# Optimization experiments

Hardware: AMD Instinct MI355X
Metric: run time of the kernel (lower is better)

Reference implementation:

```python
import jax, jax.numpy as jnp
import numpy as np

N_NODES = 100000
N_EDGES = 1600000
D_FEAT = 32


def setup_inputs() -> dict:
    key = jax.random.key(0)
    k1, k2, k3 = jax.random.split(key, 3)
    return {
        "x_real": jax.random.normal(k1, (N_NODES, D_FEAT), dtype=jnp.float32),
        "x_imag": jax.random.normal(k2, (N_NODES, D_FEAT), dtype=jnp.float32),
        "edge_index": jax.random.randint(k3, (2, N_EDGES), 0, N_NODES, dtype=jnp.int64),
        "evolution_time": jnp.asarray(0.5, dtype=jnp.float32),
        "diffusion_strength": jnp.asarray(1.0, dtype=jnp.float32),
    }


def reference(x_real, x_imag, edge_index, evolution_time, diffusion_strength):
    eps = 1e-8
    num_nodes = x_real.shape[0]
    x = x_real + 1j * x_imag  # [N, D] complex64

    # add self loops
    loops = jnp.arange(num_nodes, dtype=edge_index.dtype)
    row = jnp.concatenate([edge_index[0], loops])  # [E+N]
    col = jnp.concatenate([edge_index[1], loops])  # [E+N]

    # symmetric degree normalization: deg computed over col (as in source)
    deg = jnp.zeros((num_nodes,), jnp.float32).at[col].add(1.0)
    deg_inv_sqrt = jnp.where(deg > 0, deg ** -0.5, 0.0)
    norm = (deg_inv_sqrt[row] * deg_inv_sqrt[col])[:, None]  # [E+N, 1]

    def propagate(h):
        # gather by col, scale, scatter-add by row
        msgs = h[col] * norm.astype(h.dtype)
        return jnp.zeros_like(h).at[row].add(msgs)

    first_order = propagate(x)
    coeff1 = 1j * (evolution_time * diffusion_strength)
    evolved = x + coeff1 * first_order

    # evolution_order >= 2 (second-order Taylor term)
    second_order = propagate(first_order)
    evolved = evolved + (coeff1 * coeff1) * 0.5 * second_order

    # per-node |psi|^2 weights, normalized to sum to num_nodes
    w = (evolved * jnp.conj(evolved)).real.sum(axis=-1, keepdims=True)  # [N,1]
    s = w.sum()
    w = jnp.where(s > eps, w / s * num_nodes, jnp.ones_like(w))
    return w, evolved
```

## Files before the change

kernel.cpp:

```cpp
#include <hip/hip_runtime.h>
#include <cstdint>
#include <cstddef>


#define TPB 256
#define BSL 64
#define CRANGE 16384
#define SRANGE 8192

typedef _Float16 h2 __attribute__((ext_vector_type(2)));

#if defined(__has_builtin)
#if __has_builtin(__builtin_amdgcn_fdot2)
#define HAS_FDOT2 1
#endif
#endif

__device__ __forceinline__ h2 u2h(uint32_t u) {
    union { uint32_t u; h2 h; } x; x.u = u; return x.h;
}
__device__ __forceinline__ uint32_t h2u(h2 h) {
    union { uint32_t u; h2 h; } x; x.h = h; return x.u;
}
__device__ __forceinline__ uint32_t packh(float re, float im) {
    h2 h; h.x = (_Float16)re; h.y = (_Float16)im; return h2u(h);
}
__device__ __forceinline__ void acc2(uint32_t p, float& aR, float& aI) {
#ifdef HAS_FDOT2
    h2 v = u2h(p);
    h2 LO; LO.x = (_Float16)1.0f; LO.y = (_Float16)0.0f;
    h2 HI; HI.x = (_Float16)0.0f; HI.y = (_Float16)1.0f;
    aR = __builtin_amdgcn_fdot2(v, LO, aR, false);
    aI = __builtin_amdgcn_fdot2(v, HI, aI, false);
#else
    h2 v = u2h(p);
    aR += (float)v.x;
    aI += (float)v.y;
#endif
}

__device__ __forceinline__ int slice_len(int E) {
    return (((E + BSL - 1) / BSL) + 3) & ~3;
}

__global__ void k_cnt2(const int* __restrict__ col, const int* __restrict__ row,
                       int E, int Nw, uint32_t* __restrict__ parts_col,
                       uint32_t* __restrict__ parts_row) {
    __shared__ uint32_t sh[CRANGE / 2];
    int which = blockIdx.x & 1;
    int rb = blockIdx.x >> 1;
    int r = rb / BSL, b = rb % BSL;
    const int* keys = which ? row : col;
    uint32_t*  parts = which ? parts_row : parts_col;
    int rbase = r * CRANGE;
    for (int i = threadIdx.x; i < CRANGE / 2; i += TPB) sh[i] = 0;
    __syncthreads();
    int SL = slice_len(E);
    int s0 = b * SL, s1 = min(E, s0 + SL);
    int n = s1 - s0;
    if (n > 0) {
        const int4* k4 = (const int4*)(keys + s0);
        int n4 = n >> 2;
        for (int j = threadIdx.x; j < n4; j += TPB) {
            int4 v = k4[j];
            int k;
            k = v.x - rbase; if ((unsigned)k < CRANGE) atomicAdd(&sh[k >> 1], 1u << ((k & 1) * 16));
            k = v.y - rbase; if ((unsigned)k < CRANGE) atomicAdd(&sh[k >> 1], 1u << ((k & 1) * 16));
            k = v.z - rbase; if ((unsigned)k < CRANGE) atomicAdd(&sh[k >> 1], 1u << ((k & 1) * 16));
            k = v.w - rbase; if ((unsigned)k < CRANGE) atomicAdd(&sh[k >> 1], 1u << ((k & 1) * 16));
        }
        for (int e = s0 + (n4 << 2) + threadIdx.x; e < s1; e += TPB) {
            int k = keys[e] - rbase;
            if ((unsigned)k < CRANGE) atomicAdd(&sh[k >> 1], 1u << ((k & 1) * 16));
        }
    }
    __syncthreads();
    int wbase = rbase >> 1;
    for (int i = threadIdx.x; i < CRANGE / 2; i += TPB) {
        int w = wbase + i;
        if (w < Nw) parts[(size_t)b * Nw + w] = sh[i];
    }
}

__global__ void k_discol(const uint32_t* __restrict__ parts, int Nw, int N,
                         float* __restrict__ dis) {
    int w = blockIdx.x * blockDim.x + threadIdx.x;
    if (w >= Nw) return;
    uint32_t lo = 0, hi = 0;
    for (int b = 0; b < BSL; ++b) {
        uint32_t v = parts[(size_t)b * Nw + w];
        lo += v & 0xFFFFu; hi += v >> 16;
    }
    int n = 2 * w;
    if (n < N)     dis[n]     = rsqrtf((float)lo + 1.0f);
    if (n + 1 < N) dis[n + 1] = rsqrtf((float)hi + 1.0f);
}

__global__ void k_redrow(const uint32_t* __restrict__ parts, int Nw, int N,
                         unsigned char* __restrict__ sliceoff,
                         int* __restrict__ rowcnt) {
    int w = blockIdx.x * blockDim.x + threadIdx.x;
    if (w >= Nw) return;
    uint32_t lo = 0, hi = 0;
    int n = 2 * w;
    for (int b = 0; b < BSL; ++b) {
        uint32_t v = parts[(size_t)b * Nw + w];
        if (n < N)     sliceoff[(size_t)b * N + n]     = (unsigned char)lo;
        if (n + 1 < N) sliceoff[(size_t)b * N + n + 1] = (unsigned char)hi;
        lo += v & 0xFFFFu; hi += v >> 16;
    }
    if (n < N)     rowcnt[n]     = (int)lo;
    if (n + 1 < N) rowcnt[n + 1] = (int)hi;
}

__global__ void k_scan1(const int* __restrict__ in, int* __restrict__ out,
                        int* __restrict__ partials, int N) {
    __shared__ int sh[256];
    int t = threadIdx.x;
    int base = blockIdx.x * 1024 + t * 4;
    int v0 = (base + 0 < N) ? in[base + 0] : 0;
    int v1 = (base + 1 < N) ? in[base + 1] : 0;
    int v2 = (base + 2 < N) ? in[base + 2] : 0;
    int v3 = (base + 3 < N) ? in[base + 3] : 0;
    int s = v0 + v1 + v2 + v3;
    sh[t] = s;
    __syncthreads();
    for (int off = 1; off < 256; off <<= 1) {
        int add = (t >= off) ? sh[t - off] : 0;
        __syncthreads();
        sh[t] += add;
        __syncthreads();
    }
    int excl = sh[t] - s;
    if (base + 0 < N) out[base + 0] = excl;
    excl += v0;
    if (base + 1 < N) out[base + 1] = excl;
    excl += v1;
    if (base + 2 < N) out[base + 2] = excl;
    excl += v2;
    if (base + 3 < N) out[base + 3] = excl;
    if (t == 255) partials[blockIdx.x] = sh[255];
}

__global__ void k_scan2(int* __restrict__ partials, int nb) {
    if (threadIdx.x == 0 && blockIdx.x == 0) {
        int acc = 0;
        for (int i = 0; i < nb; ++i) { int v = partials[i]; partials[i] = acc; acc += v; }
    }
}

__global__ void k_scan3(int* __restrict__ out, const int* __restrict__ partials,
                        int N, int E) {
    int i = blockIdx.x * blockDim.x + threadIdx.x;
    if (i < N) out[i] += partials[i >> 10];
    if (i == 0) out[N] = E;
}

__global__ void k_scatter2(const int* __restrict__ row, const int* __restrict__ col,
                           int E, int N, const int* __restrict__ rowptr,
                           const unsigned char* __restrict__ sliceoff,
                           int* __restrict__ ecol) {
    __shared__ int cur[SRANGE];
    int r = blockIdx.x / BSL, b = blockIdx.x % BSL;
    int rbase = r * SRANGE;
    for (int i = threadIdx.x; i < SRANGE; i += TPB) {
        int n = rbase + i;
        cur[i] = (n < N) ? rowptr[n] + (int)sliceoff[(size_t)b * N + n] : 0;
    }
    __syncthreads();
    int SL = slice_len(E);
    int s0 = b * SL, s1 = min(E, s0 + SL);
    int n = s1 - s0;
    if (n <= 0) return;
    const int4* r4 = (const int4*)(row + s0);
    const int4* c4 = (const int4*)(col + s0);
    int n4 = n >> 2;
    for (int j = threadIdx.x; j < n4; j += TPB) {
        int4 rv = r4[j];
        int4 cv = c4[j];
        int rr;
        rr = rv.x - rbase; if ((unsigned)rr < SRANGE) ecol[atomicAdd(&cur[rr], 1)] = cv.x;
        rr = rv.y - rbase; if ((unsigned)rr < SRANGE) ecol[atomicAdd(&cur[rr], 1)] = cv.y;
        rr = rv.z - rbase; if ((unsigned)rr < SRANGE) ecol[atomicAdd(&cur[rr], 1)] = cv.z;
        rr = rv.w - rbase; if ((unsigned)rr < SRANGE) ecol[atomicAdd(&cur[rr], 1)] = cv.w;
    }
    for (int e = s0 + (n4 << 2) + threadIdx.x; e < s1; e += TPB) {
        int rr = row[e] - rbase;
        if ((unsigned)rr < SRANGE) ecol[atomicAdd(&cur[rr], 1)] = col[e];
    }
}

__global__ void k_pack(const float* __restrict__ xr, const float* __restrict__ xi,
                       const float* __restrict__ dis, uint32_t* __restrict__ xds,
                       int N) {
    int i = blockIdx.x * blockDim.x + threadIdx.x;
    if (i < N * 32) {
        int n = i >> 5, k = i & 31, s = k >> 3, dd = k & 7;
        float dg = dis[n];
        xds[((size_t)s * N + n) * 8 + dd] = packh(xr[i] * dg, xi[i] * dg);
    }
}

__device__ __forceinline__ void edge_accum8(const int* __restrict__ ecol,
                                            const uint32_t* __restrict__ hb,
                                            int beg, int end, int dd,
                                            float& aR, float& aI) {
    for (int base = beg; base < end; base += 16) {
        int m = end - base;
        int c0 = (dd < m)     ? ecol[base + dd]     : -1;
        int c1 = (8 + dd < m) ? ecol[base + 8 + dd] : -1;
        int cc[16];
        uint32_t p[16];
        #pragma unroll
        for (int k = 0; k < 8; ++k) {
            cc[k]     = __shfl(c0, k, 8);
            cc[k + 8] = __shfl(c1, k, 8);
        }
        #pragma unroll
        for (int k = 0; k < 16; ++k) {
            int c = cc[k] < 0 ? 0 : cc[k];
            uint32_t v = hb[(size_t)c * 8 + dd];
            p[k] = (cc[k] < 0) ? 0u : v;
        }
        #pragma unroll
        for (int k = 0; k < 16; ++k) acc2(p[k], aR, aI);
    }
}

__global__ void k_p1(const int* __restrict__ rowptr, const int* __restrict__ ecol,
                     const float* __restrict__ dis, const uint32_t* __restrict__ xds,
                     uint32_t* __restrict__ fo2b, uint32_t* __restrict__ fods, int N) {
    int s  = blockIdx.x & 3;
    int nb = blockIdx.x >> 2;
    int r  = nb * 32 + (threadIdx.x >> 3);
    int dd = threadIdx.x & 7;
    if (r >= N) return;
    const uint32_t* hb = xds + (size_t)s * N * 8;
    int beg = rowptr[r], end = rowptr[r + 1];
    float dg = dis[r];
    float aR = 0.f, aI = 0.f;
    edge_accum8(ecol, hb, beg, end, dd, aR, aI);
    acc2(hb[(size_t)r * 8 + dd], aR, aI);
    float foR = dg * aR, foI = dg * aI;
    size_t o = (size_t)s * N * 8 + (size_t)r * 8 + dd;
    fo2b[o] = packh(foR, foI);
    fods[o] = packh(foR * dg, foI * dg);
}

__global__ void k_p2(const int* __restrict__ rowptr, const int* __restrict__ ecol,
                     const float* __restrict__ dis, const uint32_t* __restrict__ fo2b,
                     const uint32_t* __restrict__ fods,
                     const float* __restrict__ tptr, const float* __restrict__ dptr,
                     uint32_t* __restrict__ delta, int N) {
    int s  = blockIdx.x & 3;
    int nb = blockIdx.x >> 2;
    int r  = nb * 32 + (threadIdx.x >> 3);
    int dd = threadIdx.x & 7;
    if (r >= N) return;
    const uint32_t* hb = fods + (size_t)s * N * 8;
    int beg = rowptr[r], end = rowptr[r + 1];
    float dg = dis[r];
    float aR = 0.f, aI = 0.f;
    edge_accum8(ecol, hb, beg, end, dd, aR, aI);
    acc2(hb[(size_t)r * 8 + dd], aR, aI);
    float soR = dg * aR, soI = dg * aI;
    size_t o = (size_t)s * N * 8 + (size_t)r * 8 + dd;
    h2 f = u2h(fo2b[o]);
    float foR = (float)f.x, foI = (float)f.y;
    float c1  = tptr[0] * dptr[0];
    float c2h = 0.5f * c1 * c1;
    delta[o] = packh(-c1 * foI - c2h * soR, c1 * foR - c2h * soI);
}

__global__ void k_final(const float* __restrict__ xr, const float* __restrict__ xi,
                        const uint32_t* __restrict__ delta, float* __restrict__ out,
                        int N, int interleaved, float* __restrict__ partials2) {
    int t = blockIdx.x * blockDim.x + threadIdx.x;
    int n = t >> 2, s = t & 3;
    float wsum = 0.f;
    if (n < N) {
        const uint4* dp = (const uint4*)(delta + ((size_t)s * N + n) * 8);
        uint4 d0 = dp[0], d1 = dp[1];
        size_t ib = (size_t)n * 32 + (size_t)s * 8;
        const float4* xr4 = (const float4*)(xr + ib);
        const float4* xi4 = (const float4*)(xi + ib);
        float4 a0 = xr4[0], a1 = xr4[1];
        float4 b0 = xi4[0], b1 = xi4[1];
        uint32_t dv[8] = {d0.x, d0.y, d0.z, d0.w, d1.x, d1.y, d1.z, d1.w};
        float ar[8] = {a0.x, a0.y, a0.z, a0.w, a1.x, a1.y, a1.z, a1.w};
        float ai[8] = {b0.x, b0.y, b0.z, b0.w, b1.x, b1.y, b1.z, b1.w};
        float er[8], ei[8];
        #pragma unroll
        for (int k = 0; k < 8; ++k) {
            h2 d = u2h(dv[k]);
            er[k] = ar[k] + (float)d.x;
            ei[k] = ai[k] + (float)d.y;
            wsum += er[k] * er[k] + ei[k] * ei[k];
        }
        if (interleaved) {
            float4* op = (float4*)(out + N + 2 * ib);
            op[0] = make_float4(er[0], ei[0], er[1], ei[1]);
            op[1] = make_float4(er[2], ei[2], er[3], ei[3]);
            op[2] = make_float4(er[4], ei[4], er[5], ei[5]);
            op[3] = make_float4(er[6], ei[6], er[7], ei[7]);
        } else {
            float4* op = (float4*)(out + N + ib);
            op[0] = make_float4(er[0], er[1], er[2], er[3]);
            op[1] = make_float4(er[4], er[5], er[6], er[7]);
        }
    }
    float nodesum = wsum;
    nodesum += __shfl_xor(nodesum, 1, 4);
    nodesum += __shfl_xor(nodesum, 2, 4);
    if (n < N && s == 0) out[n] = nodesum;
    float bv = wsum;
    #pragma unroll
    for (int off = 32; off; off >>= 1) bv += __shfl_xor(bv, off, 64);
    __shared__ float ls[TPB / 64];
    if ((threadIdx.x & 63) == 0) ls[threadIdx.x >> 6] = bv;
    __syncthreads();
    if (threadIdx.x == 0) {
        float bs = 0.f;
        #pragma unroll
        for (int i = 0; i < TPB / 64; ++i) bs += ls[i];
        partials2[blockIdx.x] = bs;
    }
}

__global__ void k_sum(const float* __restrict__ partials2, int nb,
                      float* __restrict__ S) {
    float acc = 0.f;
    for (int i = threadIdx.x; i < nb; i += blockDim.x) acc += partials2[i];
    #pragma unroll
    for (int off = 32; off; off >>= 1) acc += __shfl_xor(acc, off, 64);
    __shared__ float ls[TPB / 64];
    if ((threadIdx.x & 63) == 0) ls[threadIdx.x >> 6] = acc;
    __syncthreads();
    if (threadIdx.x == 0) {
        float s = 0.f;
        #pragma unroll
        for (int i = 0; i < TPB / 64; ++i) s += ls[i];
        *S = s;
    }
}

__global__ void k_norm(float* __restrict__ w, int N, const float* __restrict__ S) {
    int i = blockIdx.x * blockDim.x + threadIdx.x;
    if (i >= N) return;
    float s = *S;
    w[i] = (s > 1e-8f) ? w[i] * ((float)N / s) : 1.0f;
}

extern "C" void kernel_launch(void* const* d_in, const int* in_sizes, int n_in,
                              void* d_out, int out_size, void* d_ws, size_t ws_size,
                              hipStream_t stream) {
    const float* xr   = (const float*)d_in[0];
    const float* xi   = (const float*)d_in[1];
    const int*   eidx = (const int*)d_in[2];
    const float* tptr = (const float*)d_in[3];
    const float* dptr = (const float*)d_in[4];

    const int N = in_sizes[0] / 32;
    const int E = in_sizes[2] / 2;
    const int* row = eidx;
    const int* col = eidx + E;
    const long long ND = (long long)N * 32;
    const int Nw  = (N + 1) / 2;
    const int NB  = (N + 1023) / 1024;
    const int NBK = (N + 31) / 32;
    const int NFB = (int)((ND / 8 + TPB - 1) / TPB);
    const int NCR = (N + CRANGE - 1) / CRANGE;
    const int NSR = (N + SRANGE - 1) / SRANGE;

    size_t o = 0;
    auto alloc = [&](size_t words) {
        o = (o + 3) & ~(size_t)3;
        size_t r = o; o += words; return r;
    };
    uint32_t* wsw = (uint32_t*)d_ws;
    uint32_t*      parts_row = wsw + alloc((size_t)BSL * Nw);
    uint32_t*      parts_col = wsw + alloc((size_t)BSL * Nw);
    unsigned char* sliceoff  = (unsigned char*)(wsw + alloc(((size_t)BSL * N + 3) / 4));
    int*           rowcnt    = (int*)(wsw + alloc(N));
    int*           rowptr    = (int*)(wsw + alloc(N + 1));
    int*           partials  = (int*)(wsw + alloc(NB));
    float*         dis       = (float*)(wsw + alloc(N));
    uint32_t*      xds       = wsw + alloc(ND);
    uint32_t*      fo2b      = wsw + alloc(ND);
    uint32_t*      fods      = wsw + alloc(ND);
    float*         partials2 = (float*)(wsw + alloc(NFB));
    float*         S         = (float*)(wsw + alloc(1));
    uint32_t*      delta     = parts_row;
    int*           ecol      = (int*)parts_col;

    int interleaved = (out_size >= (int)(N + 2 * ND)) ? 1 : 0;
    float* out = (float*)d_out;

    k_cnt2<<<NCR * BSL * 2, TPB, 0, stream>>>(col, row, E, Nw, parts_col, parts_row);
    k_discol<<<(Nw + TPB - 1) / TPB, TPB, 0, stream>>>(parts_col, Nw, N, dis);
    k_redrow<<<(Nw + TPB - 1) / TPB, TPB, 0, stream>>>(parts_row, Nw, N,
                                                       sliceoff, rowcnt);
    k_scan1<<<NB, TPB, 0, stream>>>(rowcnt, rowptr, partials, N);
    k_scan2<<<1, 64, 0, stream>>>(partials, NB);
    k_scan3<<<(N + TPB - 1) / TPB, TPB, 0, stream>>>(rowptr, partials, N, E);
    k_scatter2<<<NSR * BSL, TPB, 0, stream>>>(row, col, E, N, rowptr,
                                              sliceoff, ecol);

    k_pack<<<(int)((ND + TPB - 1) / TPB), TPB, 0, stream>>>(xr, xi, dis, xds, N);
    int pgrid = 4 * NBK;
    k_p1<<<pgrid, TPB, 0, stream>>>(rowptr, ecol, dis, xds, fo2b, fods, N);
    k_p2<<<pgrid, TPB, 0, stream>>>(rowptr, ecol, dis, fo2b, fods, tptr, dptr,
                                    delta, N);
    k_final<<<NFB, TPB, 0, stream>>>(xr, xi, delta, out, N, interleaved, partials2);
    k_sum<<<1, TPB, 0, stream>>>(partials2, NFB, S);
    k_norm<<<(N + TPB - 1) / TPB, TPB, 0, stream>>>(out, N, S);
}
```

Baseline: 209.0 us.

## Gather 16-byte feature chunks per edge and split edges across lanes

```diff
diff --git a/kernel.cpp b/kernel.cpp
--- a/kernel.cpp
+++ b/kernel.cpp
@@ -37,6 +37,12 @@
     aR += (float)v.x;
     aI += (float)v.y;
 #endif
+}
+__device__ __forceinline__ void acc4(uint4 p, float (&aR)[4], float (&aI)[4]) {
+    acc2(p.x, aR[0], aI[0]);
+    acc2(p.y, aR[1], aI[1]);
+    acc2(p.z, aR[2], aI[2]);
+    acc2(p.w, aR[3], aI[3]);
 }
 
 __device__ __forceinline__ int slice_len(int E) {
@@ -201,50 +207,82 @@
     }
 }
 
-__device__ __forceinline__ void edge_accum8(const int* __restrict__ ecol,
-                                            const uint32_t* __restrict__ hb,
-                                            int beg, int end, int dd,
-                                            float& aR, float& aI) {
-    for (int base = beg; base < end; base += 16) {
-        int m = end - base;
-        int c0 = (dd < m)     ? ecol[base + dd]     : -1;
-        int c1 = (8 + dd < m) ? ecol[base + 8 + dd] : -1;
-        int cc[16];
-        uint32_t p[16];
-        #pragma unroll
-        for (int k = 0; k < 8; ++k) {
-            cc[k]     = __shfl(c0, k, 8);
-            cc[k + 8] = __shfl(c1, k, 8);
-        }
-        #pragma unroll
-        for (int k = 0; k < 16; ++k) {
-            int c = cc[k] < 0 ? 0 : cc[k];
-            uint32_t v = hb[(size_t)c * 8 + dd];
-            p[k] = (cc[k] < 0) ? 0u : v;
-        }
-        #pragma unroll
-        for (int k = 0; k < 16; ++k) acc2(p[k], aR, aI);
+__device__ __forceinline__ void edge_accum4(const int* __restrict__ ecol,
+                                            const uint4* __restrict__ hb4,
+                                            int beg, int end, int epos, int half,
+                                            float (&aR)[4], float (&aI)[4]) {
+    int base = beg;
+    for (; base + 16 <= end; base += 16) {
+        int c0 = ecol[base + epos];
+        int c1 = ecol[base + epos + 4];
+        int c2 = ecol[base + epos + 8];
+        int c3 = ecol[base + epos + 12];
+        uint4 p0 = hb4[(size_t)c0 * 2 + half];
+        uint4 p1 = hb4[(size_t)c1 * 2 + half];
+        uint4 p2 = hb4[(size_t)c2 * 2 + half];
+        uint4 p3 = hb4[(size_t)c3 * 2 + half];
+        acc4(p0, aR, aI); acc4(p1, aR, aI);
+        acc4(p2, aR, aI); acc4(p3, aR, aI);
+    }
+    if (base + 8 <= end) {
+        int c0 = ecol[base + epos];
+        int c1 = ecol[base + epos + 4];
+        uint4 p0 = hb4[(size_t)c0 * 2 + half];
+        uint4 p1 = hb4[(size_t)c1 * 2 + half];
+        acc4(p0, aR, aI); acc4(p1, aR, aI);
+        base += 8;
+    }
+    int rem = end - base;
+    if (epos < rem) {
+        int c = ecol[base + epos];
+        uint4 p = hb4[(size_t)c * 2 + half];
+        acc4(p, aR, aI);
+    }
+    if (epos + 4 < rem) {
+        int c = ecol[base + epos + 4];
+        uint4 p = hb4[(size_t)c * 2 + half];
+        acc4(p, aR, aI);
+    }
+}
+
+__device__ __forceinline__ void reduce8(float (&aR)[4], float (&aI)[4]) {
+    #pragma unroll
+    for (int d = 0; d < 4; ++d) {
+        aR[d] += __shfl_xor(aR[d], 2, 8);
+        aI[d] += __shfl_xor(aI[d], 2, 8);
+        aR[d] += __shfl_xor(aR[d], 4, 8);
+        aI[d] += __shfl_xor(aI[d], 4, 8);
     }
 }
 
 __global__ void k_p1(const int* __restrict__ rowptr, const int* __restrict__ ecol,
                      const float* __restrict__ dis, const uint32_t* __restrict__ xds,
                      uint32_t* __restrict__ fo2b, uint32_t* __restrict__ fods, int N) {
-    int s  = blockIdx.x & 3;
-    int nb = blockIdx.x >> 2;
-    int r  = nb * 32 + (threadIdx.x >> 3);
-    int dd = threadIdx.x & 7;
+    int s   = blockIdx.x & 3;
+    int nb  = blockIdx.x >> 2;
+    int r   = nb * 32 + (threadIdx.x >> 3);
+    int sub = threadIdx.x & 7;
+    int half = sub & 1, epos = sub >> 1;
     if (r >= N) return;
-    const uint32_t* hb = xds + (size_t)s * N * 8;
+    const uint4* hb4 = (const uint4*)(xds + (size_t)s * N * 8);
     int beg = rowptr[r], end = rowptr[r + 1];
     float dg = dis[r];
-    float aR = 0.f, aI = 0.f;
-    edge_accum8(ecol, hb, beg, end, dd, aR, aI);
-    acc2(hb[(size_t)r * 8 + dd], aR, aI);
-    float foR = dg * aR, foI = dg * aI;
-    size_t o = (size_t)s * N * 8 + (size_t)r * 8 + dd;
-    fo2b[o] = packh(foR, foI);
-    fods[o] = packh(foR * dg, foI * dg);
+    float aR[4] = {0.f, 0.f, 0.f, 0.f}, aI[4] = {0.f, 0.f, 0.f, 0.f};
+    edge_accum4(ecol, hb4, beg, end, epos, half, aR, aI);
+    reduce8(aR, aI);
+    acc4(hb4[(size_t)r * 2 + half], aR, aI);
+    if (epos == 0) {
+        float foR[4], foI[4];
+        #pragma unroll
+        for (int d = 0; d < 4; ++d) { foR[d] = dg * aR[d]; foI[d] = dg * aI[d]; }
+        uint4 f, fd;
+        f.x = packh(foR[0], foI[0]); f.y = packh(foR[1], foI[1]);
+        f.z = packh(foR[2], foI[2]); f.w = packh(foR[3], foI[3]);
+        fd.x = packh(foR[0] * dg, foI[0] * dg); fd.y = packh(foR[1] * dg, foI[1] * dg);
+        fd.z = packh(foR[2] * dg, foI[2] * dg); fd.w = packh(foR[3] * dg, foI[3] * dg);
+        ((uint4*)(fo2b + (size_t)s * N * 8))[(size_t)r * 2 + half] = f;
+        ((uint4*)(fods + (size_t)s * N * 8))[(size_t)r * 2 + half] = fd;
+    }
 }
 
 __global__ void k_p2(const int* __restrict__ rowptr, const int* __restrict__ ecol,
@@ -252,24 +290,36 @@
                      const uint32_t* __restrict__ fods,
                      const float* __restrict__ tptr, const float* __restrict__ dptr,
                      uint32_t* __restrict__ delta, int N) {
-    int s  = blockIdx.x & 3;
-    int nb = blockIdx.x >> 2;
-    int r  = nb * 32 + (threadIdx.x >> 3);
-    int dd = threadIdx.x & 7;
+    int s   = blockIdx.x & 3;
+    int nb  = blockIdx.x >> 2;
+    int r   = nb * 32 + (threadIdx.x >> 3);
+    int sub = threadIdx.x & 7;
+    int half = sub & 1, epos = sub >> 1;
     if (r >= N) return;
-    const uint32_t* hb = fods + (size_t)s * N * 8;
+    const uint4* hb4 = (const uint4*)(fods + (size_t)s * N * 8);
     int beg = rowptr[r], end = rowptr[r + 1];
     float dg = dis[r];
-    float aR = 0.f, aI = 0.f;
-    edge_accum8(ecol, hb, beg, end, dd, aR, aI);
-    acc2(hb[(size_t)r * 8 + dd], aR, aI);
-    float soR = dg * aR, soI = dg * aI;
-    size_t o = (size_t)s * N * 8 + (size_t)r * 8 + dd;
-    h2 f = u2h(fo2b[o]);
-    float foR = (float)f.x, foI = (float)f.y;
-    float c1  = tptr[0] * dptr[0];
-    float c2h = 0.5f * c1 * c1;
-    delta[o] = packh(-c1 * foI - c2h * soR, c1 * foR - c2h * soI);
+    float aR[4] = {0.f, 0.f, 0.f, 0.f}, aI[4] = {0.f, 0.f, 0.f, 0.f};
+    edge_accum4(ecol, hb4, beg, end, epos, half, aR, aI);
+    reduce8(aR, aI);
+    acc4(hb4[(size_t)r * 2 + half], aR, aI);
+    if (epos == 0) {
+        float c1  = tptr[0] * dptr[0];
+        float c2h = 0.5f * c1 * c1;
+        uint4 f = ((const uint4*)(fo2b + (size_t)s * N * 8))[(size_t)r * 2 + half];
+        uint32_t fv[4] = {f.x, f.y, f.z, f.w};
+        uint4 dlt;
+        uint32_t dv[4];
+        #pragma unroll
+        for (int d = 0; d < 4; ++d) {
+            float soR = dg * aR[d], soI = dg * aI[d];
+            h2 fo = u2h(fv[d]);
+            float foR = (float)fo.x, foI = (float)fo.y;
+            dv[d] = packh(-c1 * foI - c2h * soR, c1 * foR - c2h * soI);
+        }
+        dlt.x = dv[0]; dlt.y = dv[1]; dlt.z = dv[2]; dlt.w = dv[3];
+        ((uint4*)(delta + (size_t)s * N * 8))[(size_t)r * 2 + half] = dlt;
+    }
 }
 
 __global__ void k_final(const float* __restrict__ xr, const float* __restrict__ xi,
```

After: 211.4 us. No clear change (+1.1%).
